# Kernel optimization log

Measured on AMD Instinct MI355X. Metric: run time of the kernel, lower is better.

The kernel has to match this reference:

```python
import jax, jax.numpy as jnp
import numpy as np

DROPOUT_P = 0.1  # original source passed p=1 (degenerate, zeros output); 0.1 used for a meaningful baseline


def setup_inputs() -> dict:
    key0 = jax.random.key(0)
    ks = jax.random.split(key0, 11)
    B, H, L, D, DQK, DV = 2, 8, 2048, 1024, 64, 64
    return {
        "query": jax.random.normal(ks[0], (B, H, L, D), jnp.float32),
        "key":   jax.random.normal(ks[1], (B, H, L, D), jnp.float32),
        "value": jax.random.normal(ks[2], (B, H, L, D), jnp.float32),
        "Wq": jax.random.normal(ks[3], (D, DQK), jnp.float32) * (D ** -0.5),
        "bq": jax.random.normal(ks[4], (DQK,), jnp.float32) * 0.02,
        "Wk": jax.random.normal(ks[5], (D, DQK), jnp.float32) * (D ** -0.5),
        "bk": jax.random.normal(ks[6], (DQK,), jnp.float32) * 0.02,
        "Wv": jax.random.normal(ks[7], (D, DV), jnp.float32) * (D ** -0.5),
        "bv": jax.random.normal(ks[8], (DV,), jnp.float32) * 0.02,
        "Wo": jax.random.normal(ks[9], (DV, D), jnp.float32) * (DV ** -0.5),
        "bo": jax.random.normal(ks[10], (D,), jnp.float32) * 0.02,
    }


def reference(query, key, value, Wq, bq, Wk, bk, Wv, bv, Wo, bo):
    # Per-head linear projections on 4D inputs (B,H,L,d_model)
    q = query @ Wq + bq            # (B,H,Lq,dqk)
    k = key @ Wk + bk              # (B,H,Lk,dqk)
    v = value @ Wv + bv            # (B,H,Lk,dv)
    # Quirky scale from source: q.size(2)*q.size(3)/key.size(2) * key.size(-1)**-0.5
    dk = (q.shape[2] * q.shape[3] / key.shape[2]) * (key.shape[-1] ** -0.5)
    scores = jnp.einsum('bhqd,bhkd->bhqk', q, k) * jnp.float32(dk)
    attn = jax.nn.softmax(scores, axis=-1)
    # Deterministic dropout with fixed key (inverted-scale, matching F.dropout)
    keep = jax.random.bernoulli(jax.random.key(42), 1.0 - DROPOUT_P, attn.shape)
    attn = jnp.where(keep, attn / (1.0 - DROPOUT_P), jnp.float32(0.0))
    out = jnp.einsum('bhqk,bhkd->bhqd', attn, v)  # (B,H,Lq,dv)
    return out @ Wo + bo                           # (B,H,Lq,d_model)
```

## Files before the change

kernel.cpp:

```cpp
#include <hip/hip_runtime.h>
#include <stdint.h>

typedef _Float16 f16;
typedef __attribute__((ext_vector_type(8))) _Float16 f16x8;
typedef __attribute__((ext_vector_type(4))) float f32x4;

__device__ __forceinline__ uint32_t rotl1(uint32_t x, uint32_t n){
  return __builtin_amdgcn_alignbit(x, x, 32u - n);
}
__device__ __forceinline__ uint32_t tf_bits(uint32_t i){
  const uint32_t ks1 = 42u, ks2 = 0x1BD11BDAu ^ 42u;
  uint32_t x0 = 0u, x1 = i + 42u;
#define R4(a,b,c,d) \
  x0 += x1; x1 = rotl1(x1,a); x1 ^= x0; \
  x0 += x1; x1 = rotl1(x1,b); x1 ^= x0; \
  x0 += x1; x1 = rotl1(x1,c); x1 ^= x0; \
  x0 += x1; x1 = rotl1(x1,d); x1 ^= x0;
  R4(13,15,26,6)  x0 += ks1; x1 += ks2 + 1u;
  R4(17,29,16,24) x0 += ks2; x1 += 2u;
  R4(13,15,26,6)               x1 += ks1 + 3u;
  R4(17,29,16,24) x0 += ks1; x1 += ks2 + 4u;
  R4(13,15,26,6)  x0 += ks2; x1 += 5u;
#undef R4
  return x0 ^ x1;
}

template<int PACKED>
__global__ __launch_bounds__(256) void proj_kernel(
    const float* __restrict__ query, const float* __restrict__ keyp, const float* __restrict__ value,
    const float* __restrict__ Wq, const float* __restrict__ bq,
    const float* __restrict__ Wk, const float* __restrict__ bk,
    const float* __restrict__ Wv, const float* __restrict__ bv,
    const float* __restrict__ Wo,
    f16* __restrict__ qp, f16* __restrict__ kp, f16* __restrict__ vpT,
    f16* __restrict__ WoT)
{
  __shared__ __align__(16) f16 Alds[64][40];
  __shared__ __align__(16) f16 Wlds[64][40];
  const int bid = blockIdx.x;
  const int tid = threadIdx.x;
  const int lane = tid & 63, wave = tid >> 6;
  const int llo = lane & 15, lhi = lane >> 4;

  int p;
  if (PACKED == 0){
    if (bid < 256){
      int t = bid*256 + tid;
      int n = t & 1023, k = t >> 10;
      WoT[(long)n*64 + k] = (f16)Wo[(long)k*1024 + n];
      return;
    }
    p = bid - 256;
  } else {
    p = 768 + bid;
  }

  const int which = p >> 9;
  const long m0 = (long)(p & 511) * 64;
  const float* A    = which==0 ? query : (which==1 ? keyp : value);
  const float* W    = which==0 ? Wq    : (which==1 ? Wk   : Wv);
  const float* bias = which==0 ? bq    : (which==1 ? bk   : bv);

  f32x4 acc[4];
  #pragma unroll
  for (int n=0;n<4;n++){
    float bb = bias[16*n + llo];
    acc[n][0]=bb; acc[n][1]=bb; acc[n][2]=bb; acc[n][3]=bb;
  }

  const int ar = tid >> 2;
  const int ac = (tid & 3) * 8;
  const int wcol = tid & 63;
  const int wk = (tid >> 6) * 8;

  for (int k0 = 0; k0 < 1024; k0 += 32){
    {
      const float* asrc = A + (m0 + ar)*1024 + k0 + ac;
      float4 v0 = *(const float4*)asrc;
      float4 v1 = *(const float4*)(asrc + 4);
      if (PACKED == 0){
        f16* ad = &Alds[ar][ac];
        ad[0]=(f16)v0.x; ad[1]=(f16)v0.y; ad[2]=(f16)v0.z; ad[3]=(f16)v0.w;
        ad[4]=(f16)v1.x; ad[5]=(f16)v1.y; ad[6]=(f16)v1.z; ad[7]=(f16)v1.w;
      } else {
        union { f16 h[8]; f16x8 v; } aw;
        aw.h[0]=(f16)v0.x; aw.h[1]=(f16)v0.y; aw.h[2]=(f16)v0.z; aw.h[3]=(f16)v0.w;
        aw.h[4]=(f16)v1.x; aw.h[5]=(f16)v1.y; aw.h[6]=(f16)v1.z; aw.h[7]=(f16)v1.w;
        *(f16x8*)&Alds[ar][ac] = aw.v;
      }
      f16 wt[8];
      #pragma unroll
      for (int j=0;j<8;j++) wt[j] = (f16)W[(long)(k0+wk+j)*64 + wcol];
      *(f16x8*)&Wlds[wcol][wk] = *(f16x8*)wt;
    }
    __syncthreads();
    f16x8 af = *(const f16x8*)&Alds[wave*16 + llo][lhi*8];
    #pragma unroll
    for (int n=0;n<4;n++){
      f16x8 bf = *(const f16x8*)&Wlds[16*n + llo][lhi*8];
      acc[n] = __builtin_amdgcn_mfma_f32_16x16x32_f16(af, bf, acc[n], 0,0,0);
    }
    __syncthreads();
  }

  if (which < 2){
    const float scale = (which==0) ? 2.0f : 1.0f;
    f16* dst = (which==0) ? qp : kp;
    #pragma unroll
    for (int n=0;n<4;n++)
      #pragma unroll
      for (int j=0;j<4;j++){
        long row = m0 + wave*16 + lhi*4 + j;
        dst[row*64 + 16*n + llo] = (f16)(acc[n][j]*scale);
      }
  } else {
    long row0 = m0 + wave*16 + lhi*4;
    long bh = row0 >> 11;
    long lr = row0 & 2047;
    #pragma unroll
    for (int n=0;n<4;n++){
      union { f16 h[4]; ushort4 u; } pk;
      #pragma unroll
      for (int j=0;j<4;j++) pk.h[j] = (f16)acc[n][j];
      *(ushort4*)&vpT[(bh*64 + 16*n + llo)*2048 + lr] = pk.u;
    }
  }
}

__global__ __launch_bounds__(256) void flash_kernel(
    const f16* __restrict__ qp, const f16* __restrict__ kp, const f16* __restrict__ vpT,
    const f16* __restrict__ WoT, const float* __restrict__ bo, float* __restrict__ out)
{
  __shared__ __align__(16) f16 Klds[64][72];
  __shared__ __align__(16) f16 Vlds[64][72];
  __shared__ __align__(16) f16 Plds[4][16][72];
  __shared__ unsigned short Idl[4][1024];
  const int tid = threadIdx.x;
  const int lane = tid & 63, wave = tid >> 6;
  const int llo = lane & 15, lhi = lane >> 4;
  const int bh = blockIdx.y;
  const int q0 = blockIdx.x * 64;

  const f16* qbase = qp + ((long)bh*2048 + q0 + wave*16 + llo)*64 + lhi*8;
  f16x8 qf0 = *(const f16x8*)qbase;
  f16x8 qf1 = *(const f16x8*)(qbase + 32);

  f32x4 O[4];
  float mrun[4], lrun[4];
  #pragma unroll
  for (int n=0;n<4;n++){ O[n][0]=0.f;O[n][1]=0.f;O[n][2]=0.f;O[n][3]=0.f; }
  #pragma unroll
  for (int j=0;j<4;j++){ mrun[j] = -__builtin_inff(); lrun[j]=0.f; }

  const int sr = tid >> 2;
  const int sc = (tid & 3) * 16;
  const f16* kbh = kp + (long)bh*2048*64;
  const f16* vbh = vpT + (long)bh*64*2048;
  uint32_t base_w = (uint32_t)((bh*2048 + q0 + wave*16)*2048);

  for (int kv0 = 0; kv0 < 2048; kv0 += 64, base_w += 64u){
    {
      const f16* src = kbh + (long)(kv0 + sr)*64 + sc;
      f16x8 t0 = *(const f16x8*)src;
      f16x8 t1 = *(const f16x8*)(src+8);
      *(f16x8*)&Klds[sr][sc]   = t0;
      *(f16x8*)&Klds[sr][sc+8] = t1;
      const f16* vsrc = vbh + (long)sr*2048 + kv0 + sc;
      f16x8 u0 = *(const f16x8*)vsrc;
      f16x8 u1 = *(const f16x8*)(vsrc+8);
      *(f16x8*)&Vlds[sr][sc]   = u0;
      *(f16x8*)&Vlds[sr][sc+8] = u1;
    }
    __syncthreads();

    f32x4 s[4];
    #pragma unroll
    for (int n=0;n<4;n++){ s[n][0]=0.f;s[n][1]=0.f;s[n][2]=0.f;s[n][3]=0.f; }
    #pragma unroll
    for (int n=0;n<4;n++){
      f16x8 kf0 = *(const f16x8*)&Klds[16*n+llo][lhi*8];
      s[n] = __builtin_amdgcn_mfma_f32_16x16x32_f16(qf0, kf0, s[n], 0,0,0);
      f16x8 kf1 = *(const f16x8*)&Klds[16*n+llo][32+lhi*8];
      s[n] = __builtin_amdgcn_mfma_f32_16x16x32_f16(qf1, kf1, s[n], 0,0,0);
    }
    float pmax[4];
    #pragma unroll
    for (int j=0;j<4;j++)
      pmax[j] = fmaxf(fmaxf(s[0][j],s[1][j]), fmaxf(s[2][j],s[3][j]));
    #pragma unroll
    for (int off=1; off<16; off<<=1){
      #pragma unroll
      for (int j=0;j<4;j++) pmax[j] = fmaxf(pmax[j], __shfl_xor(pmax[j], off));
    }
    float esc[4];
    #pragma unroll
    for (int j=0;j<4;j++){
      float mnew = fmaxf(mrun[j], pmax[j]);
      esc[j] = __expf(mrun[j] - mnew);
      mrun[j] = mnew;
    }
    float p[4][4]; float lsum[4] = {0.f,0.f,0.f,0.f};
    #pragma unroll
    for (int n=0;n<4;n++)
      #pragma unroll
      for (int j=0;j<4;j++){
        p[n][j] = __expf(s[n][j] - mrun[j]);
        lsum[j] += p[n][j];
      }
    #pragma unroll
    for (int off=1; off<16; off<<=1){
      #pragma unroll
      for (int j=0;j<4;j++) lsum[j] += __shfl_xor(lsum[j], off);
    }
    #pragma unroll
    for (int j=0;j<4;j++) lrun[j] = lrun[j]*esc[j] + lsum[j];
    #pragma unroll
    for (int n=0;n<4;n++)
      #pragma unroll
      for (int j=0;j<4;j++) O[n][j] *= esc[j];

    uint32_t cnt = 0;
    #pragma unroll
    for (int j=0;j<4;j++){
      #pragma unroll
      for (int n=0;n<4;n++){
        float pm = p[n][j]*(1.0f/0.9f);
        bool surv = pm > 0x1.0p-25f;
        Plds[wave][lhi*4+j][16*n+llo] = (f16)pm;
        unsigned long long mk = __ballot(surv);
        if (mk){
          uint32_t pre = __builtin_amdgcn_mbcnt_hi((uint32_t)(mk>>32),
                         __builtin_amdgcn_mbcnt_lo((uint32_t)mk, 0u));
          if (surv)
            Idl[wave][cnt + pre] = (unsigned short)((j<<8)|(n<<6)|lane);
          cnt += (uint32_t)__builtin_popcountll(mk);
        }
      }
    }
    for (uint32_t pb = 0; pb < cnt; pb += 64){
      uint32_t idx = pb + (uint32_t)lane;
      if (idx < cnt){
        uint32_t id = (uint32_t)Idl[wave][idx];
        uint32_t jj = (id>>8)&3u, nn = (id>>6)&3u, ln = id & 63u;
        uint32_t i = base_w + (ln>>4)*8192u + jj*2048u + nn*16u + (ln&15u);
        uint32_t bits = tf_bits(i);
        if (bits >= 0xE6666600u)
          Plds[wave][(ln>>4)*4+jj][16*nn+(ln&15u)] = (f16)0;
      }
    }

    f16x8 pa0 = *(const f16x8*)&Plds[wave][llo][lhi*8];
    f16x8 pa1 = *(const f16x8*)&Plds[wave][llo][32+lhi*8];
    #pragma unroll
    for (int n=0;n<4;n++){
      f16x8 vf0 = *(const f16x8*)&Vlds[16*n+llo][lhi*8];
      O[n] = __builtin_amdgcn_mfma_f32_16x16x32_f16(pa0, vf0, O[n], 0,0,0);
      f16x8 vf1 = *(const f16x8*)&Vlds[16*n+llo][32+lhi*8];
      O[n] = __builtin_amdgcn_mfma_f32_16x16x32_f16(pa1, vf1, O[n], 0,0,0);
    }
    __syncthreads();
  }

  float rl[4];
  #pragma unroll
  for (int j=0;j<4;j++) rl[j] = 1.0f / lrun[j];
  #pragma unroll
  for (int n=0;n<4;n++)
    #pragma unroll
    for (int j=0;j<4;j++)
      Klds[wave*16 + lhi*4 + j][16*n + llo] = (f16)(O[n][j]*rl[j]);
  __syncthreads();

  f16x8 af0 = *(const f16x8*)&Klds[wave*16 + llo][lhi*8];
  f16x8 af1 = *(const f16x8*)&Klds[wave*16 + llo][32 + lhi*8];
  const long robase = (long)bh*2048 + q0 + wave*16 + lhi*4;
  for (int n0 = 0; n0 < 1024; n0 += 16){
    f16x8 b0 = *(const f16x8*)&WoT[(long)(n0+llo)*64 + lhi*8];
    f16x8 b1 = *(const f16x8*)&WoT[(long)(n0+llo)*64 + 32 + lhi*8];
    float bb = bo[n0+llo];
    f32x4 c; c[0]=bb; c[1]=bb; c[2]=bb; c[3]=bb;
    c = __builtin_amdgcn_mfma_f32_16x16x32_f16(af0, b0, c, 0,0,0);
    c = __builtin_amdgcn_mfma_f32_16x16x32_f16(af1, b1, c, 0,0,0);
    #pragma unroll
    for (int j=0;j<4;j++)
      out[(robase + j)*1024 + n0 + llo] = c[j];
  }
}

extern "C" void kernel_launch(void* const* d_in, const int* in_sizes, int n_in,
                              void* d_out, int out_size, void* d_ws, size_t ws_size,
                              hipStream_t stream){
  const float* query = (const float*)d_in[0];
  const float* key   = (const float*)d_in[1];
  const float* value = (const float*)d_in[2];
  const float* Wq = (const float*)d_in[3];
  const float* bq = (const float*)d_in[4];
  const float* Wk = (const float*)d_in[5];
  const float* bk = (const float*)d_in[6];
  const float* Wv = (const float*)d_in[7];
  const float* bv = (const float*)d_in[8];
  const float* Wo = (const float*)d_in[9];
  const float* bo = (const float*)d_in[10];
  float* out = (float*)d_out;

  char* ws = (char*)d_ws;
  f16* qp   = (f16*)(ws);
  f16* kp   = (f16*)(ws + ((size_t)4<<20));
  f16* vpT  = (f16*)(ws + ((size_t)8<<20));
  f16* WoT  = (f16*)(ws + ((size_t)20<<20));

  proj_kernel<0><<<dim3(1024), dim3(256), 0, stream>>>(
      query,key,value,Wq,bq,Wk,bk,Wv,bv,Wo,qp,kp,vpT,WoT);
  proj_kernel<1><<<dim3(768), dim3(256), 0, stream>>>(
      query,key,value,Wq,bq,Wk,bk,Wv,bv,Wo,qp,kp,vpT,WoT);
  flash_kernel<<<dim3(32,16), dim3(256), 0, stream>>>(qp,kp,vpT,WoT,bo,out);
}
```

Measured before the change: 247.7 us.

## Split KV range across two blocks and add separate combine+output-projection kernel

The flash kernel now splits the 2048-long key/value range into two halves via a z grid dimension, doubling the number of blocks from 512 to 1024 to better fill the GPU. Each half writes unnormalized fp32 partial outputs plus running max and sum to workspace. A new combine kernel merges the two partials with log-sum-exp weights and performs the Wo projection plus bias, parallelized over output-column chunks. This adds extra global traffic for partials and one more kernel launch, and the combine kernel reloads partial rows per column chunk.

Measured after the change: 257.9 us. +4.1%, slower.

```diff
diff --git a/kernel.cpp b/kernel.cpp
--- a/kernel.cpp
+++ b/kernel.cpp
@@ -129,7 +129,7 @@
 
 __global__ __launch_bounds__(256) void flash_kernel(
     const f16* __restrict__ qp, const f16* __restrict__ kp, const f16* __restrict__ vpT,
-    const f16* __restrict__ WoT, const float* __restrict__ bo, float* __restrict__ out)
+    float* __restrict__ Opart, float* __restrict__ Mp, float* __restrict__ Lp)
 {
   __shared__ __align__(16) f16 Klds[64][72];
   __shared__ __align__(16) f16 Vlds[64][72];
@@ -140,6 +140,7 @@
   const int llo = lane & 15, lhi = lane >> 4;
   const int bh = blockIdx.y;
   const int q0 = blockIdx.x * 64;
+  const int kvh = blockIdx.z;
 
   const f16* qbase = qp + ((long)bh*2048 + q0 + wave*16 + llo)*64 + lhi*8;
   f16x8 qf0 = *(const f16x8*)qbase;
@@ -156,9 +157,10 @@
   const int sc = (tid & 3) * 16;
   const f16* kbh = kp + (long)bh*2048*64;
   const f16* vbh = vpT + (long)bh*64*2048;
-  uint32_t base_w = (uint32_t)((bh*2048 + q0 + wave*16)*2048);
-
-  for (int kv0 = 0; kv0 < 2048; kv0 += 64, base_w += 64u){
+  uint32_t base_w = (uint32_t)((bh*2048 + q0 + wave*16)*2048) + (uint32_t)(kvh*1024);
+
+  const int kvlo = kvh*1024, kvhi = kvlo + 1024;
+  for (int kv0 = kvlo; kv0 < kvhi; kv0 += 64, base_w += 64u){
     {
       const f16* src = kbh + (long)(kv0 + sr)*64 + sc;
       f16x8 t0 = *(const f16x8*)src;
@@ -261,20 +263,54 @@
     __syncthreads();
   }
 
-  float rl[4];
-  #pragma unroll
-  for (int j=0;j<4;j++) rl[j] = 1.0f / lrun[j];
+  const long pr = ((long)kvh*16 + bh)*2048 + q0 + wave*16 + lhi*4;
   #pragma unroll
   for (int n=0;n<4;n++)
     #pragma unroll
     for (int j=0;j<4;j++)
-      Klds[wave*16 + lhi*4 + j][16*n + llo] = (f16)(O[n][j]*rl[j]);
-  __syncthreads();
-
-  f16x8 af0 = *(const f16x8*)&Klds[wave*16 + llo][lhi*8];
-  f16x8 af1 = *(const f16x8*)&Klds[wave*16 + llo][32 + lhi*8];
-  const long robase = (long)bh*2048 + q0 + wave*16 + lhi*4;
-  for (int n0 = 0; n0 < 1024; n0 += 16){
+      Opart[(pr + j)*64 + 16*n + llo] = O[n][j];
+  if (llo == 0){
+    const long mr = (long)kvh*32768 + bh*2048 + q0 + wave*16 + lhi*4;
+    #pragma unroll
+    for (int j=0;j<4;j++){ Mp[mr + j] = mrun[j]; Lp[mr + j] = lrun[j]; }
+  }
+}
+
+__global__ __launch_bounds__(256) void combine_kernel(
+    const float* __restrict__ Opart, const float* __restrict__ Mp, const float* __restrict__ Lp,
+    const f16* __restrict__ WoT, const float* __restrict__ bo, float* __restrict__ out)
+{
+  const int tid = threadIdx.x;
+  const int lane = tid & 63, wave = tid >> 6;
+  const int llo = lane & 15, lhi = lane >> 4;
+  const long m0 = (long)blockIdx.x * 64;
+  const int nb = blockIdx.y * 256;
+
+  const long gr = m0 + wave*16 + llo;
+  float m0v = Mp[gr], m1v = Mp[32768 + gr];
+  float l0  = Lp[gr], l1  = Lp[32768 + gr];
+  float M  = fmaxf(m0v, m1v);
+  float e0 = __expf(m0v - M), e1 = __expf(m1v - M);
+  float rl = 1.0f / (l0*e0 + l1*e1);
+  float w0 = e0*rl, w1 = e1*rl;
+
+  const float* o0 = Opart + gr*64;
+  const float* o1 = Opart + 2097152 + gr*64;
+  f16x8 af0, af1;
+  {
+    union { f16 h[8]; f16x8 v; } u;
+    const int c0 = lhi*8;
+    #pragma unroll
+    for (int e=0;e<8;e++) u.h[e] = (f16)(o0[c0+e]*w0 + o1[c0+e]*w1);
+    af0 = u.v;
+    const int c1 = 32 + lhi*8;
+    #pragma unroll
+    for (int e=0;e<8;e++) u.h[e] = (f16)(o0[c1+e]*w0 + o1[c1+e]*w1);
+    af1 = u.v;
+  }
+
+  const long robase = m0 + wave*16 + lhi*4;
+  for (int n0 = nb; n0 < nb+256; n0 += 16){
     f16x8 b0 = *(const f16x8*)&WoT[(long)(n0+llo)*64 + lhi*8];
     f16x8 b1 = *(const f16x8*)&WoT[(long)(n0+llo)*64 + 32 + lhi*8];
     float bb = bo[n0+llo];
@@ -304,14 +340,18 @@
   float* out = (float*)d_out;
 
   char* ws = (char*)d_ws;
-  f16* qp   = (f16*)(ws);
-  f16* kp   = (f16*)(ws + ((size_t)4<<20));
-  f16* vpT  = (f16*)(ws + ((size_t)8<<20));
-  f16* WoT  = (f16*)(ws + ((size_t)20<<20));
+  f16* qp      = (f16*)(ws);
+  f16* kp      = (f16*)(ws + ((size_t)4<<20));
+  f16* vpT     = (f16*)(ws + ((size_t)8<<20));
+  float* Opart = (float*)(ws + ((size_t)12<<20));
+  float* Mp    = (float*)(ws + ((size_t)28<<20));
+  float* Lp    = (float*)(ws + ((size_t)28<<20) + (256<<10));
+  f16* WoT     = (f16*)(ws + ((size_t)28<<20) + (512<<10));
 
   proj_kernel<0><<<dim3(1024), dim3(256), 0, stream>>>(
       query,key,value,Wq,bq,Wk,bk,Wv,bv,Wo,qp,kp,vpT,WoT);
   proj_kernel<1><<<dim3(768), dim3(256), 0, stream>>>(
       query,key,value,Wq,bq,Wk,bk,Wv,bv,Wo,qp,kp,vpT,WoT);
-  flash_kernel<<<dim3(32,16), dim3(256), 0, stream>>>(qp,kp,vpT,WoT,bo,out);
-}
+  flash_kernel<<<dim3(32,16,2), dim3(256), 0, stream>>>(qp,kp,vpT,Opart,Mp,Lp);
+  combine_kernel<<<dim3(512,4), dim3(256), 0, stream>>>(Opart,Mp,Lp,WoT,bo,out);
+}
```

## Split flash attention KV range across two blocks with ticket-based merge

Applied to the files above, without the earlier changes.

Doubles the flash kernel grid by splitting the 2048-key range into two halves along blockIdx.z. Each half writes partial O, running max and running sum to workspace. An atomic ticket lets the second finisher merge both partials with softmax rescaling and then do the output projection. This targets low occupancy (512 blocks on a large GPU) at the cost of extra global traffic for the partials, an extra memset, and a fence and atomic per block.

New measurement: 403.3 us. +62.8%, slower.

```diff
diff --git a/kernel.cpp b/kernel.cpp
--- a/kernel.cpp
+++ b/kernel.cpp
@@ -129,17 +129,21 @@
 
 __global__ __launch_bounds__(256) void flash_kernel(
     const f16* __restrict__ qp, const f16* __restrict__ kp, const f16* __restrict__ vpT,
+    float* __restrict__ Opart, float* __restrict__ Mp, float* __restrict__ Lp,
+    unsigned int* __restrict__ ticket,
     const f16* __restrict__ WoT, const float* __restrict__ bo, float* __restrict__ out)
 {
   __shared__ __align__(16) f16 Klds[64][72];
   __shared__ __align__(16) f16 Vlds[64][72];
   __shared__ __align__(16) f16 Plds[4][16][72];
   __shared__ unsigned short Idl[4][1024];
+  __shared__ unsigned int sOld;
   const int tid = threadIdx.x;
   const int lane = tid & 63, wave = tid >> 6;
   const int llo = lane & 15, lhi = lane >> 4;
   const int bh = blockIdx.y;
   const int q0 = blockIdx.x * 64;
+  const int kvh = blockIdx.z;
 
   const f16* qbase = qp + ((long)bh*2048 + q0 + wave*16 + llo)*64 + lhi*8;
   f16x8 qf0 = *(const f16x8*)qbase;
@@ -156,9 +160,10 @@
   const int sc = (tid & 3) * 16;
   const f16* kbh = kp + (long)bh*2048*64;
   const f16* vbh = vpT + (long)bh*64*2048;
-  uint32_t base_w = (uint32_t)((bh*2048 + q0 + wave*16)*2048);
-
-  for (int kv0 = 0; kv0 < 2048; kv0 += 64, base_w += 64u){
+  uint32_t base_w = (uint32_t)((bh*2048 + q0 + wave*16)*2048) + (uint32_t)(kvh*1024);
+
+  const int kvlo = kvh*1024, kvhi = kvlo + 1024;
+  for (int kv0 = kvlo; kv0 < kvhi; kv0 += 64, base_w += 64u){
     {
       const f16* src = kbh + (long)(kv0 + sr)*64 + sc;
       f16x8 t0 = *(const f16x8*)src;
@@ -261,14 +266,44 @@
     __syncthreads();
   }
 
-  float rl[4];
-  #pragma unroll
-  for (int j=0;j<4;j++) rl[j] = 1.0f / lrun[j];
-  #pragma unroll
-  for (int n=0;n<4;n++)
-    #pragma unroll
-    for (int j=0;j<4;j++)
-      Klds[wave*16 + lhi*4 + j][16*n + llo] = (f16)(O[n][j]*rl[j]);
+  const long rbase = (long)bh*2048 + q0 + wave*16 + lhi*4;
+  {
+    const long pr = (long)kvh*2097152 + rbase*64;
+    #pragma unroll
+    for (int n=0;n<4;n++)
+      #pragma unroll
+      for (int j=0;j<4;j++)
+        Opart[pr + (long)j*64 + 16*n + llo] = O[n][j];
+    if (llo == 0){
+      const long mr = (long)kvh*32768 + rbase;
+      #pragma unroll
+      for (int j=0;j<4;j++){ Mp[mr + j] = mrun[j]; Lp[mr + j] = lrun[j]; }
+    }
+  }
+  __threadfence();
+  if (tid == 0) sOld = atomicAdd(&ticket[bh*32 + blockIdx.x], 1u);
+  __syncthreads();
+  if (sOld == 0u) return;
+  __threadfence();
+
+  const int zo = kvh ^ 1;
+  {
+    const long mro = (long)zo*32768 + rbase;
+    const long pro = (long)zo*2097152 + rbase*64;
+    #pragma unroll
+    for (int j=0;j<4;j++){
+      float mo = Mp[mro + j], lo = Lp[mro + j];
+      float M  = fmaxf(mrun[j], mo);
+      float ew = __expf(mrun[j] - M), eo = __expf(mo - M);
+      float rl = 1.0f / (lrun[j]*ew + lo*eo);
+      float wW = ew*rl, wO = eo*rl;
+      #pragma unroll
+      for (int n=0;n<4;n++){
+        float oo = Opart[pro + (long)j*64 + 16*n + llo];
+        Klds[wave*16 + lhi*4 + j][16*n + llo] = (f16)(O[n][j]*wW + oo*wO);
+      }
+    }
+  }
   __syncthreads();
 
   f16x8 af0 = *(const f16x8*)&Klds[wave*16 + llo][lhi*8];
@@ -304,14 +339,20 @@
   float* out = (float*)d_out;
 
   char* ws = (char*)d_ws;
-  f16* qp   = (f16*)(ws);
-  f16* kp   = (f16*)(ws + ((size_t)4<<20));
-  f16* vpT  = (f16*)(ws + ((size_t)8<<20));
-  f16* WoT  = (f16*)(ws + ((size_t)20<<20));
-
+  f16* qp      = (f16*)(ws);
+  f16* kp      = (f16*)(ws + ((size_t)4<<20));
+  f16* vpT     = (f16*)(ws + ((size_t)8<<20));
+  float* Opart = (float*)(ws + ((size_t)12<<20));
+  float* Mp    = (float*)(ws + ((size_t)28<<20));
+  float* Lp    = (float*)(ws + ((size_t)28<<20) + (256<<10));
+  f16* WoT     = (f16*)(ws + ((size_t)28<<20) + (512<<10));
+  unsigned int* ticket = (unsigned int*)(ws + ((size_t)28<<20) + (768<<10));
+
+  hipMemsetAsync(ticket, 0, 512*sizeof(unsigned int), stream);
   proj_kernel<0><<<dim3(1024), dim3(256), 0, stream>>>(
       query,key,value,Wq,bq,Wk,bk,Wv,bv,Wo,qp,kp,vpT,WoT);
   proj_kernel<1><<<dim3(768), dim3(256), 0, stream>>>(
       query,key,value,Wq,bq,Wk,bk,Wv,bv,Wo,qp,kp,vpT,WoT);
-  flash_kernel<<<dim3(32,16), dim3(256), 0, stream>>>(qp,kp,vpT,WoT,bo,out);
-}
+  flash_kernel<<<dim3(32,16,2), dim3(256), 0, stream>>>(
+      qp,kp,vpT,Opart,Mp,Lp,ticket,WoT,bo,out);
+}
```

## Double-buffer K/V tiles in LDS with register prefetch in flash kernel

Applied to the files above, without the earlier changes.

Each loop iteration now issues the global loads for the next K/V tile into registers before the QK^T, softmax and dropout work, and writes them into the alternate LDS buffer after the PV MMA. This removes one __syncthreads per iteration and hides global load latency behind compute. In exchange it doubles the K/V LDS footprint, which may lower occupancy, and adds eight f16x8 registers of prefetch state per thread.

Measured after the change: 252.0 us. Within noise of the previous version (+1.7%).

```diff
diff --git a/kernel.cpp b/kernel.cpp
--- a/kernel.cpp
+++ b/kernel.cpp
@@ -131,8 +131,8 @@
     const f16* __restrict__ qp, const f16* __restrict__ kp, const f16* __restrict__ vpT,
     const f16* __restrict__ WoT, const float* __restrict__ bo, float* __restrict__ out)
 {
-  __shared__ __align__(16) f16 Klds[64][72];
-  __shared__ __align__(16) f16 Vlds[64][72];
+  __shared__ __align__(16) f16 Klds[2][64][72];
+  __shared__ __align__(16) f16 Vlds[2][64][72];
   __shared__ __align__(16) f16 Plds[4][16][72];
   __shared__ unsigned short Idl[4][1024];
   const int tid = threadIdx.x;
@@ -154,33 +154,39 @@
 
   const int sr = tid >> 2;
   const int sc = (tid & 3) * 16;
-  const f16* kbh = kp + (long)bh*2048*64;
-  const f16* vbh = vpT + (long)bh*64*2048;
+  const f16* ksrc = kp + (long)bh*2048*64 + (long)sr*64 + sc;
+  const f16* vsrc = vpT + (long)bh*64*2048 + (long)sr*2048 + sc;
   uint32_t base_w = (uint32_t)((bh*2048 + q0 + wave*16)*2048);
 
-  for (int kv0 = 0; kv0 < 2048; kv0 += 64, base_w += 64u){
-    {
-      const f16* src = kbh + (long)(kv0 + sr)*64 + sc;
-      f16x8 t0 = *(const f16x8*)src;
-      f16x8 t1 = *(const f16x8*)(src+8);
-      *(f16x8*)&Klds[sr][sc]   = t0;
-      *(f16x8*)&Klds[sr][sc+8] = t1;
-      const f16* vsrc = vbh + (long)sr*2048 + kv0 + sc;
-      f16x8 u0 = *(const f16x8*)vsrc;
-      f16x8 u1 = *(const f16x8*)(vsrc+8);
-      *(f16x8*)&Vlds[sr][sc]   = u0;
-      *(f16x8*)&Vlds[sr][sc+8] = u1;
-    }
-    __syncthreads();
+  f16x8 kr0 = *(const f16x8*)(ksrc);
+  f16x8 kr1 = *(const f16x8*)(ksrc + 8);
+  f16x8 vr0 = *(const f16x8*)(vsrc);
+  f16x8 vr1 = *(const f16x8*)(vsrc + 8);
+  *(f16x8*)&Klds[0][sr][sc]   = kr0;
+  *(f16x8*)&Klds[0][sr][sc+8] = kr1;
+  *(f16x8*)&Vlds[0][sr][sc]   = vr0;
+  *(f16x8*)&Vlds[0][sr][sc+8] = vr1;
+  __syncthreads();
+
+  for (int t = 0; t < 32; ++t, base_w += 64u){
+    const int buf = t & 1;
+    if (t < 31){
+      const f16* ks = ksrc + (long)(t+1)*4096;
+      kr0 = *(const f16x8*)ks;
+      kr1 = *(const f16x8*)(ks + 8);
+      const f16* vs = vsrc + (long)(t+1)*64;
+      vr0 = *(const f16x8*)vs;
+      vr1 = *(const f16x8*)(vs + 8);
+    }
 
     f32x4 s[4];
     #pragma unroll
     for (int n=0;n<4;n++){ s[n][0]=0.f;s[n][1]=0.f;s[n][2]=0.f;s[n][3]=0.f; }
     #pragma unroll
     for (int n=0;n<4;n++){
-      f16x8 kf0 = *(const f16x8*)&Klds[16*n+llo][lhi*8];
+      f16x8 kf0 = *(const f16x8*)&Klds[buf][16*n+llo][lhi*8];
       s[n] = __builtin_amdgcn_mfma_f32_16x16x32_f16(qf0, kf0, s[n], 0,0,0);
-      f16x8 kf1 = *(const f16x8*)&Klds[16*n+llo][32+lhi*8];
+      f16x8 kf1 = *(const f16x8*)&Klds[buf][16*n+llo][32+lhi*8];
       s[n] = __builtin_amdgcn_mfma_f32_16x16x32_f16(qf1, kf1, s[n], 0,0,0);
     }
     float pmax[4];
@@ -253,11 +259,18 @@
     f16x8 pa1 = *(const f16x8*)&Plds[wave][llo][32+lhi*8];
     #pragma unroll
     for (int n=0;n<4;n++){
-      f16x8 vf0 = *(const f16x8*)&Vlds[16*n+llo][lhi*8];
+      f16x8 vf0 = *(const f16x8*)&Vlds[buf][16*n+llo][lhi*8];
       O[n] = __builtin_amdgcn_mfma_f32_16x16x32_f16(pa0, vf0, O[n], 0,0,0);
-      f16x8 vf1 = *(const f16x8*)&Vlds[16*n+llo][32+lhi*8];
+      f16x8 vf1 = *(const f16x8*)&Vlds[buf][16*n+llo][32+lhi*8];
       O[n] = __builtin_amdgcn_mfma_f32_16x16x32_f16(pa1, vf1, O[n], 0,0,0);
     }
+
+    if (t < 31){
+      *(f16x8*)&Klds[buf^1][sr][sc]   = kr0;
+      *(f16x8*)&Klds[buf^1][sr][sc+8] = kr1;
+      *(f16x8*)&Vlds[buf^1][sr][sc]   = vr0;
+      *(f16x8*)&Vlds[buf^1][sr][sc+8] = vr1;
+    }
     __syncthreads();
   }
 
@@ -268,11 +281,11 @@
   for (int n=0;n<4;n++)
     #pragma unroll
     for (int j=0;j<4;j++)
-      Klds[wave*16 + lhi*4 + j][16*n + llo] = (f16)(O[n][j]*rl[j]);
+      Klds[0][wave*16 + lhi*4 + j][16*n + llo] = (f16)(O[n][j]*rl[j]);
   __syncthreads();
 
-  f16x8 af0 = *(const f16x8*)&Klds[wave*16 + llo][lhi*8];
-  f16x8 af1 = *(const f16x8*)&Klds[wave*16 + llo][32 + lhi*8];
+  f16x8 af0 = *(const f16x8*)&Klds[0][wave*16 + llo][lhi*8];
+  f16x8 af1 = *(const f16x8*)&Klds[0][wave*16 + llo][32 + lhi*8];
   const long robase = (long)bh*2048 + q0 + wave*16 + lhi*4;
   for (int n0 = 0; n0 < 1024; n0 += 16){
     f16x8 b0 = *(const f16x8*)&WoT[(long)(n0+llo)*64 + lhi*8];
```
